# Kernel optimization log

Measured on AMD Instinct MI355X. Metric: run time of the kernel, lower is better.

The kernel has to match this reference:

```python
import jax, jax.numpy as jnp
import numpy as np

NSAMPLES = 30
TOPK = 32
EPS = 1e-8


def setup_inputs() -> dict:
    key = jax.random.key(0)
    k1, k2 = jax.random.split(key)
    B, N, C, S = 4, 4096, 256, 256
    x = jax.random.normal(k1, (B, N, C), dtype=jnp.float32)
    # affinity matrix (B, num_spixels, N); strictly positive weights for multinomial
    amatrix = jax.random.uniform(k2, (B, S, N), dtype=jnp.float32)
    return {"x": x, "amatrix": amatrix, "num_spixels": S}


def _exact_attn(x, sims, indices, labels):
    # x: (B,N,C); sims/indices: (B,S,K) topk affinities / pixel ids per superpixel
    # labels: (B,N) sampled superpixel id per pixel
    C = x.shape[-1]
    # per-pixel gather of its sampled superpixel's top-K member pixels
    idx = jnp.take_along_axis(indices, labels[:, :, None], axis=1)   # (B,N,K)
    w = jnp.take_along_axis(sims, labels[:, :, None], axis=1)        # (B,N,K)
    keys = jax.vmap(lambda xb, ib: xb[ib])(x, idx)                   # (B,N,K,C)
    scores = jnp.einsum('bnc,bnkc->bnk', x, keys) / jnp.sqrt(jnp.float32(C))
    attn = jax.nn.softmax(scores + jnp.log(w + EPS), axis=-1)        # (B,N,K)
    return jnp.einsum('bnk,bnkc->bnc', attn, keys)


def reference(x, amatrix, num_spixels):
    # topk over candidate-pixel axis, once (torch.topk(amatrix, topk, dim=-1))
    sims, indices = jax.lax.top_k(amatrix, TOPK)                     # (B,S,K)
    # multinomial(amatrix.T): sample a superpixel per pixel from its affinity column
    logits = jnp.log(amatrix + EPS).transpose(0, 2, 1)               # (B,N,S)
    sample_keys = jax.random.split(jax.random.key(1), NSAMPLES)

    def body(acc, k):
        labels = jax.random.categorical(k, logits, axis=-1)          # (B,N)
        acc = acc + _exact_attn(x, sims, indices, labels) / NSAMPLES
        return acc, None

    out, _ = jax.lax.scan(body, jnp.zeros_like(x), sample_keys)
    return out
```

## Files before the change

kernel.cpp:

```cpp
#include <hip/hip_runtime.h>
#include <hip/hip_bf16.h>


#define BB 4
#define NN 4096
#define CC 256
#define SS 256
#define KKK 32
#define NSAMP 30
#define NBIN (BB*SS)
#define TOTQ (NSAMP*BB*NN)

typedef _Float16 half8 __attribute__((ext_vector_type(8)));
typedef _Float16 half4v __attribute__((ext_vector_type(4)));
typedef float f32x4 __attribute__((ext_vector_type(4)));

struct Keys30 { unsigned k0[NSAMP]; unsigned k1[NSAMP]; };

__host__ __device__ __forceinline__ void threefry2x32(unsigned k0, unsigned k1,
    unsigned x0, unsigned x1, unsigned& o0, unsigned& o1) {
  unsigned ks2 = k0 ^ k1 ^ 0x1BD11BDAu;
#define TFROT(r) { x0 += x1; x1 = (x1 << (r)) | (x1 >> (32 - (r))); x1 ^= x0; }
  x0 += k0; x1 += k1;
  TFROT(13) TFROT(15) TFROT(26) TFROT(6)
  x0 += k1;  x1 += ks2 + 1u;
  TFROT(17) TFROT(29) TFROT(16) TFROT(24)
  x0 += ks2; x1 += k0 + 2u;
  TFROT(13) TFROT(15) TFROT(26) TFROT(6)
  x0 += k0;  x1 += k1 + 3u;
  TFROT(17) TFROT(29) TFROT(16) TFROT(24)
  x0 += k1;  x1 += ks2 + 4u;
  TFROT(13) TFROT(15) TFROT(26) TFROT(6)
  x0 += ks2; x1 += k0 + 5u;
#undef TFROT
  o0 = x0; o1 = x1;
}

__device__ __forceinline__ float gumbel_from_bits(unsigned bits) {
  float u = __uint_as_float((bits >> 9) | 0x3f800000u) - 1.0f;
  u = fmaxf(u, 1.17549435e-38f);
  return -logf(-logf(u));
}

__global__ __launch_bounds__(256) void logit_kernel(const float* __restrict__ am,
                                                    float* __restrict__ lg) {
  int i = (blockIdx.x * 256 + threadIdx.x) << 2;
  float4 v = *(const float4*)&am[i];
  float4 o;
  o.x = logf(v.x + 1e-8f); o.y = logf(v.y + 1e-8f);
  o.z = logf(v.z + 1e-8f); o.w = logf(v.w + 1e-8f);
  *(float4*)&lg[i] = o;
}

__global__ __launch_bounds__(256) void topk_kernel(const float* __restrict__ am,
                                                   int* __restrict__ indices,
                                                   float* __restrict__ logw) {
  __shared__ float vals[NN];
  __shared__ float wv[4];
  __shared__ int   wi[4];
  const int row = blockIdx.x;
  const int tid = threadIdx.x;
  const float* src = am + (size_t)row * NN;
  for (int i = tid; i < NN; i += 256) vals[i] = src[i];
  __syncthreads();
  for (int k = 0; k < KKK; ++k) {
    float bv = -INFINITY; int bi = -1;
    #pragma unroll
    for (int j = 0; j < NN / 256; ++j) {
      int idx = tid + j * 256;
      float v = vals[idx];
      if (v > bv) { bv = v; bi = idx; }
    }
    #pragma unroll
    for (int off = 32; off; off >>= 1) {
      float ov = __shfl_down(bv, off);
      int   oi = __shfl_down(bi, off);
      if (ov > bv || (ov == bv && oi < bi)) { bv = ov; bi = oi; }
    }
    if ((tid & 63) == 0) { wv[tid >> 6] = bv; wi[tid >> 6] = bi; }
    __syncthreads();
    if (tid == 0) {
      bv = wv[0]; bi = wi[0];
      for (int w = 1; w < 4; ++w)
        if (wv[w] > bv || (wv[w] == bv && wi[w] < bi)) { bv = wv[w]; bi = wi[w]; }
      indices[row * KKK + k] = bi;
      logw[row * KKK + k] = logf(bv + 1e-8f);
      vals[bi] = -INFINITY;
    }
    __syncthreads();
  }
}

__global__ __launch_bounds__(256) void sample_part_kernel(
    const float* __restrict__ lg, unsigned char* __restrict__ labels, Keys30 keys) {
  const int t = blockIdx.x * 256 + threadIdx.x;
  const int n = t & (NN - 1);
  const int b = (t >> 12) & 3;
  const int samp = t >> 14;
  const unsigned k0 = keys.k0[samp], k1 = keys.k1[samp];
  const unsigned jbase = ((unsigned)((b << 12) + n)) << 8;
  float best = -INFINITY; int bi = 0;
  for (int s = 0; s < SS; ++s) {
    float logit = lg[((b << 8) + s) * NN + n];
    unsigned o0, o1;
    threefry2x32(k0, k1, 0u, jbase + (unsigned)s, o0, o1);
    float tot = gumbel_from_bits(o0 ^ o1) + logit;
    if (tot > best) { best = tot; bi = s; }
  }
  labels[((samp << 2) + b) * NN + n] = (unsigned char)bi;
}

__global__ __launch_bounds__(256) void hist_kernel(const unsigned char* __restrict__ lbl,
                                                   int* __restrict__ hist) {
  __shared__ int h[NBIN];
  for (int i = threadIdx.x; i < NBIN; i += 256) h[i] = 0;
  __syncthreads();
  for (int e = blockIdx.x * 256 + threadIdx.x; e < TOTQ; e += gridDim.x * 256) {
    int bgrp = (e >> 12) & 3;
    atomicAdd(&h[(bgrp << 8) + lbl[e]], 1);
  }
  __syncthreads();
  for (int i = threadIdx.x; i < NBIN; i += 256) if (h[i]) atomicAdd(&hist[i], h[i]);
}

__global__ __launch_bounds__(1024) void scan_kernel(const int* __restrict__ hist,
                                                    int* __restrict__ binstart,
                                                    int* __restrict__ cursor) {
  __shared__ int a[NBIN];
  const int tid = threadIdx.x;
  const int h = hist[tid];
  a[tid] = h;
  __syncthreads();
  for (int off = 1; off < NBIN; off <<= 1) {
    int v = (tid >= off) ? a[tid - off] : 0;
    __syncthreads();
    a[tid] += v;
    __syncthreads();
  }
  int excl = a[tid] - h;
  binstart[tid] = excl;
  cursor[tid]   = excl;
}

__global__ __launch_bounds__(256) void scatter_kernel(const unsigned char* __restrict__ lbl,
                                                      int* __restrict__ cursor,
                                                      int* __restrict__ qlist) {
  for (int e = blockIdx.x * 256 + threadIdx.x; e < TOTQ; e += gridDim.x * 256) {
    int bgrp = (e >> 12) & 3;
    int bin = (bgrp << 8) + lbl[e];
    int slot = atomicAdd(&cursor[bin], 1);
    qlist[slot] = e & (NN - 1);
  }
}

__global__ __launch_bounds__(256, 2) void attn_mfma_kernel(
    const float* __restrict__ x, const int* __restrict__ indices,
    const float* __restrict__ logw, const int* __restrict__ qlist,
    const int* __restrict__ binstart, const int* __restrict__ hist,
    float* __restrict__ out) {
  __shared__ _Float16 Qlds[64 * 256];
  __shared__ _Float16 Klds[32 * 256];
  __shared__ _Float16 KT[256 * 40];
  __shared__ _Float16 Plds[4 * 16 * 32];
  __shared__ int   kidx_s[KKK];
  __shared__ float kbias_s[KKK];

  const int tid = threadIdx.x;
  const int b = blockIdx.x & 3;
  const int s = blockIdx.x >> 2;
  const int bin = (b << 8) + s;
  const int base = binstart[bin];
  const int cnt  = hist[bin];

  if (tid < KKK) {
    int r = bin * KKK + tid;
    kidx_s[tid]  = indices[r];
    kbias_s[tid] = logw[r];
  }
  __syncthreads();

  const int w = tid >> 6, lane = tid & 63;
  const int qr = lane & 15, kg = lane >> 4;

  {
    const int c4 = (lane) << 2;
    #pragma unroll
    for (int p = 0; p < 8; ++p) {
      int r = (p << 2) + w;
      const float4 v = *(const float4*)&x[((size_t)((b << 12) + kidx_s[r]) << 8) + c4];
      half4v h;
      h[0] = (_Float16)v.x; h[1] = (_Float16)v.y;
      h[2] = (_Float16)v.z; h[3] = (_Float16)v.w;
      *(half4v*)&Klds[(r << 8) + (c4 ^ ((r & 7) << 3))] = h;
      KT[(c4 + 0) * 40 + r] = h[0];
      KT[(c4 + 1) * 40 + r] = h[1];
      KT[(c4 + 2) * 40 + r] = h[2];
      KT[(c4 + 3) * 40 + r] = h[3];
    }
  }

  const int nchunk = (cnt + 63) >> 6;
  for (int chk = 0; chk < nchunk; ++chk) {
    const int rmax = min(64, cnt - (chk << 6));
    __syncthreads();
    {
      const int c4 = lane << 2;
      #pragma unroll
      for (int p = 0; p < 16; ++p) {
        int r = (p << 2) + w;
        int rr = min(r, rmax - 1);
        int n = qlist[base + (chk << 6) + rr];
        const float4 v = *(const float4*)&x[((size_t)((b << 12) + n) << 8) + c4];
        half4v h;
        h[0] = (_Float16)v.x; h[1] = (_Float16)v.y;
        h[2] = (_Float16)v.z; h[3] = (_Float16)v.w;
        *(half4v*)&Qlds[(r << 8) + (c4 ^ ((r & 7) << 3))] = h;
      }
    }
    __syncthreads();

    f32x4 acc0 = {0.f, 0.f, 0.f, 0.f}, acc1 = {0.f, 0.f, 0.f, 0.f};
    {
      const int arow = (w << 4) + qr;
      const _Float16* Arow = &Qlds[arow << 8];
      const int asz = (arow & 7) << 3;
      const _Float16* B0 = &Klds[qr << 8];
      const _Float16* B1 = &Klds[(16 + qr) << 8];
      const int bsz = (qr & 7) << 3;
      #pragma unroll
      for (int kk = 0; kk < 8; ++kk) {
        const int off = (kk << 5) + (kg << 3);
        half8 a  = *(const half8*)&Arow[off ^ asz];
        half8 b0 = *(const half8*)&B0[off ^ bsz];
        half8 b1 = *(const half8*)&B1[off ^ bsz];
        acc0 = __builtin_amdgcn_mfma_f32_16x16x32_f16(a, b0, acc0, 0, 0, 0);
        acc1 = __builtin_amdgcn_mfma_f32_16x16x32_f16(a, b1, acc1, 0, 0, 0);
      }
    }
    {
      const float b0v = kbias_s[qr], b1v = kbias_s[16 + qr];
      #pragma unroll
      for (int r = 0; r < 4; ++r) {
        float s0 = acc0[r] * 0.0625f + b0v;
        float s1 = acc1[r] * 0.0625f + b1v;
        float m = fmaxf(s0, s1);
        #pragma unroll
        for (int o = 1; o < 16; o <<= 1) m = fmaxf(m, __shfl_xor(m, o));
        float e0 = __expf(s0 - m), e1 = __expf(s1 - m);
        float sm = e0 + e1;
        #pragma unroll
        for (int o = 1; o < 16; o <<= 1) sm += __shfl_xor(sm, o);
        float inv = 1.0f / sm;
        int prow = (kg << 2) + r;
        _Float16* P = &Plds[(w << 9) + (prow << 5)];
        P[qr]      = (_Float16)(e0 * inv);
        P[16 + qr] = (_Float16)(e1 * inv);
      }
    }
    __builtin_amdgcn_wave_barrier();
    {
      half8 a2 = *(const half8*)&Plds[(w << 9) + (qr << 5) + (kg << 3)];
      int nr[4];
      #pragma unroll
      for (int r = 0; r < 4; ++r) {
        int grow = (w << 4) + (kg << 2) + r;
        nr[r] = (grow < rmax) ? qlist[base + (chk << 6) + grow] : -1;
      }
      #pragma unroll
      for (int t = 0; t < 16; ++t) {
        half8 bb = *(const half8*)&KT[((t << 4) + qr) * 40 + (kg << 3)];
        f32x4 zero = {0.f, 0.f, 0.f, 0.f};
        f32x4 o = __builtin_amdgcn_mfma_f32_16x16x32_f16(a2, bb, zero, 0, 0, 0);
        #pragma unroll
        for (int r = 0; r < 4; ++r) {
          if (nr[r] >= 0)
            atomicAdd(&out[((size_t)((b << 12) + nr[r]) << 8) + (t << 4) + qr],
                      o[r] * (1.0f / 30.0f));
        }
      }
    }
  }
}

#define OFF_IDX   0
#define OFF_LOGW  131072
#define OFF_LBL   262144
#define OFF_LOGIT 786432
#define OFF_HIST  17563648
#define OFF_BST   17567744
#define OFF_CUR   17571840
#define OFF_QL    17575936

extern "C" void kernel_launch(void* const* d_in, const int* in_sizes, int n_in,
                              void* d_out, int out_size, void* d_ws, size_t ws_size,
                              hipStream_t stream) {
  const float* x  = (const float*)d_in[0];
  const float* am = (const float*)d_in[1];
  float* out = (float*)d_out;

  char* ws = (char*)d_ws;
  int*   indices = (int*)(ws + OFF_IDX);
  float* logw    = (float*)(ws + OFF_LOGW);
  unsigned char* labels = (unsigned char*)(ws + OFF_LBL);
  float* logits  = (float*)(ws + OFF_LOGIT);
  int*   hist    = (int*)(ws + OFF_HIST);
  int*   binstart= (int*)(ws + OFF_BST);
  int*   cursor  = (int*)(ws + OFF_CUR);
  int*   qlist   = (int*)(ws + OFF_QL);

  Keys30 keys;
  for (int s = 0; s < NSAMP; ++s) {
    unsigned o0, o1;
    threefry2x32(0u, 1u, 0u, (unsigned)s, o0, o1);
    keys.k0[s] = o0; keys.k1[s] = o1;
  }

  hipMemsetAsync(d_out, 0, (size_t)out_size * 4, stream);
  hipMemsetAsync(hist, 0, NBIN * 4, stream);

  logit_kernel<<<(BB * SS * NN) / (256 * 4), 256, 0, stream>>>(am, logits);
  topk_kernel<<<BB * SS, 256, 0, stream>>>(am, indices, logw);
  sample_part_kernel<<<TOTQ / 256, 256, 0, stream>>>(logits, labels, keys);
  hist_kernel<<<240, 256, 0, stream>>>(labels, hist);
  scan_kernel<<<1, 1024, 0, stream>>>(hist, binstart, cursor);
  scatter_kernel<<<240, 256, 0, stream>>>(labels, cursor, qlist);
  attn_mfma_kernel<<<NBIN, 256, 0, stream>>>(x, indices, logw, qlist, binstart,
                                             hist, out);
}
```

Baseline: 998.0 us.

## Screen Gumbel-max candidates with fast logs, recompute exact only near-best

The sampling kernel now scores each candidate superpixel with fast __logf Gumbel noise and keeps a running threshold. It marks only candidates within a small margin of the running best, or with extreme noise, and re-evaluates just those with exact logf to choose the argmax. This targets the cost of two precise logs per candidate across all 256 superpixels. In exchange it adds a second threefry evaluation per surviving candidate plus divergent per-wave loops, and it relies on the margin to preserve exact label selection. The rotate is also expressed as a builtin.

```diff
diff --git a/kernel.cpp b/kernel.cpp
--- a/kernel.cpp
+++ b/kernel.cpp
@@ -20,7 +20,7 @@
 __host__ __device__ __forceinline__ void threefry2x32(unsigned k0, unsigned k1,
     unsigned x0, unsigned x1, unsigned& o0, unsigned& o1) {
   unsigned ks2 = k0 ^ k1 ^ 0x1BD11BDAu;
-#define TFROT(r) { x0 += x1; x1 = (x1 << (r)) | (x1 >> (32 - (r))); x1 ^= x0; }
+#define TFROT(r) { x0 += x1; x1 = __builtin_rotateleft32(x1, (r)); x1 ^= x0; }
   x0 += k0; x1 += k1;
   TFROT(13) TFROT(15) TFROT(26) TFROT(6)
   x0 += k1;  x1 += ks2 + 1u;
@@ -36,9 +36,13 @@
   o0 = x0; o1 = x1;
 }
 
-__device__ __forceinline__ float gumbel_from_bits(unsigned bits) {
+__device__ __forceinline__ float uniform_from_bits(unsigned bits) {
   float u = __uint_as_float((bits >> 9) | 0x3f800000u) - 1.0f;
-  u = fmaxf(u, 1.17549435e-38f);
+  return fmaxf(u, 1.17549435e-38f);
+}
+
+__device__ __forceinline__ float gumbel_exact(unsigned bits) {
+  float u = uniform_from_bits(bits);
   return -logf(-logf(u));
 }
 
@@ -91,7 +95,7 @@
   }
 }
 
-__global__ __launch_bounds__(256) void sample_part_kernel(
+__global__ __launch_bounds__(256) void sample_screen_kernel(
     const float* __restrict__ lg, unsigned char* __restrict__ labels, Keys30 keys) {
   const int t = blockIdx.x * 256 + threadIdx.x;
   const int n = t & (NN - 1);
@@ -99,13 +103,40 @@
   const int samp = t >> 14;
   const unsigned k0 = keys.k0[samp], k1 = keys.k1[samp];
   const unsigned jbase = ((unsigned)((b << 12) + n)) << 8;
-  float best = -INFINITY; int bi = 0;
-  for (int s = 0; s < SS; ++s) {
-    float logit = lg[((b << 8) + s) * NN + n];
-    unsigned o0, o1;
-    threefry2x32(k0, k1, 0u, jbase + (unsigned)s, o0, o1);
-    float tot = gumbel_from_bits(o0 ^ o1) + logit;
-    if (tot > best) { best = tot; bi = s; }
+  const float* lcol = lg + ((size_t)(b << 8)) * NN + n;
+
+  const float MARGIN2 = 0.01f;
+  float thr  = -INFINITY;
+  float best = -INFINITY;
+  int   bi   = 0;
+
+  for (int grp = 0; grp < 8; ++grp) {
+    const int sbase = grp << 5;
+    unsigned m = 0;
+    #pragma unroll 4
+    for (int i = 0; i < 32; ++i) {
+      const int s = sbase + i;
+      float logit = lcol[(size_t)s * NN];
+      unsigned o0, o1;
+      threefry2x32(k0, k1, 0u, jbase + (unsigned)s, o0, o1);
+      float u  = uniform_from_bits(o0 ^ o1);
+      float gt = -__logf(-__logf(u));
+      float at = gt + logit;
+      bool force = (gt > 16.0f) || !(gt == gt);
+      if (force || at >= thr - MARGIN2) m |= (1u << i);
+      if (!force) thr = fmaxf(thr, at);
+    }
+    while (__ballot(m != 0)) {
+      if (m) {
+        int i = __builtin_ctz(m);
+        m &= m - 1;
+        int s = sbase + i;
+        unsigned o0, o1;
+        threefry2x32(k0, k1, 0u, jbase + (unsigned)s, o0, o1);
+        float tot = gumbel_exact(o0 ^ o1) + lcol[(size_t)s * NN];
+        if (tot > best) { best = tot; bi = s; }
+      }
+    }
   }
   labels[((samp << 2) + b) * NN + n] = (unsigned char)bi;
 }
@@ -320,7 +351,7 @@
 
   logit_kernel<<<(BB * SS * NN) / (256 * 4), 256, 0, stream>>>(am, logits);
   topk_kernel<<<BB * SS, 256, 0, stream>>>(am, indices, logw);
-  sample_part_kernel<<<TOTQ / 256, 256, 0, stream>>>(logits, labels, keys);
+  sample_screen_kernel<<<TOTQ / 256, 256, 0, stream>>>(logits, labels, keys);
   hist_kernel<<<240, 256, 0, stream>>>(labels, hist);
   scan_kernel<<<1, 1024, 0, stream>>>(hist, binstart, cursor);
   scatter_kernel<<<240, 256, 0, stream>>>(labels, cursor, qlist);
```

New measurement: 1.042 ms. 4.4% more time.

## Replace Gumbel double-log sampling with exponential-race using one fast log

Applied to the files above, without the earlier changes.

Sampling now uses the identity argmax(g+log w) = argmin(-log u / w), so each candidate costs one hardware log and a multiply by a precomputed -1/w, instead of two accurate logs plus a logit add. The kernel tracks the best and second-best ratio and, when the two are within a small relative margin, redoes the exact Gumbel computation so the chosen labels match the reference. The rotate macro now uses a rotate builtin. The risk is the fallback path causing wavefront divergence, and the approximate log possibly picking a different winner at ties outside the guard margin.

```diff
diff --git a/kernel.cpp b/kernel.cpp
--- a/kernel.cpp
+++ b/kernel.cpp
@@ -20,7 +20,7 @@
 __host__ __device__ __forceinline__ void threefry2x32(unsigned k0, unsigned k1,
     unsigned x0, unsigned x1, unsigned& o0, unsigned& o1) {
   unsigned ks2 = k0 ^ k1 ^ 0x1BD11BDAu;
-#define TFROT(r) { x0 += x1; x1 = (x1 << (r)) | (x1 >> (32 - (r))); x1 ^= x0; }
+#define TFROT(r) { x0 += x1; x1 = __builtin_rotateleft32(x1, (r)); x1 ^= x0; }
   x0 += k0; x1 += k1;
   TFROT(13) TFROT(15) TFROT(26) TFROT(6)
   x0 += k1;  x1 += ks2 + 1u;
@@ -36,20 +36,24 @@
   o0 = x0; o1 = x1;
 }
 
-__device__ __forceinline__ float gumbel_from_bits(unsigned bits) {
+__device__ __forceinline__ float uniform_from_bits(unsigned bits) {
   float u = __uint_as_float((bits >> 9) | 0x3f800000u) - 1.0f;
-  u = fmaxf(u, 1.17549435e-38f);
+  return fmaxf(u, 1.17549435e-38f);
+}
+
+__device__ __forceinline__ float gumbel_exact(unsigned bits) {
+  float u = uniform_from_bits(bits);
   return -logf(-logf(u));
 }
 
-__global__ __launch_bounds__(256) void logit_kernel(const float* __restrict__ am,
-                                                    float* __restrict__ lg) {
+__global__ __launch_bounds__(256) void invw_kernel(const float* __restrict__ am,
+                                                   float* __restrict__ nw) {
   int i = (blockIdx.x * 256 + threadIdx.x) << 2;
   float4 v = *(const float4*)&am[i];
   float4 o;
-  o.x = logf(v.x + 1e-8f); o.y = logf(v.y + 1e-8f);
-  o.z = logf(v.z + 1e-8f); o.w = logf(v.w + 1e-8f);
-  *(float4*)&lg[i] = o;
+  o.x = -1.0f / (v.x + 1e-8f); o.y = -1.0f / (v.y + 1e-8f);
+  o.z = -1.0f / (v.z + 1e-8f); o.w = -1.0f / (v.w + 1e-8f);
+  *(float4*)&nw[i] = o;
 }
 
 __global__ __launch_bounds__(256) void topk_kernel(const float* __restrict__ am,
@@ -91,23 +95,45 @@
   }
 }
 
-__global__ __launch_bounds__(256) void sample_part_kernel(
-    const float* __restrict__ lg, unsigned char* __restrict__ labels, Keys30 keys) {
-  const int t = blockIdx.x * 256 + threadIdx.x;
-  const int n = t & (NN - 1);
-  const int b = (t >> 12) & 3;
-  const int samp = t >> 14;
+__global__ __launch_bounds__(256) void sample_top2_kernel(
+    const float* __restrict__ ninvw, const float* __restrict__ am,
+    unsigned char* __restrict__ labels, Keys30 keys) {
+  const int t0 = blockIdx.x * 256 + threadIdx.x;
+  const int n = t0 & (NN - 1);
+  const int b = (t0 >> 12) & 3;
+  const int samp = t0 >> 14;
   const unsigned k0 = keys.k0[samp], k1 = keys.k1[samp];
   const unsigned jbase = ((unsigned)((b << 12) + n)) << 8;
-  float best = -INFINITY; int bi = 0;
+  const float* wcol = ninvw + ((size_t)(b << 8)) * NN + n;
+
+  float r1 = INFINITY, r2 = INFINITY;
+  int   i1 = 0;
+  #pragma unroll 8
   for (int s = 0; s < SS; ++s) {
-    float logit = lg[((b << 8) + s) * NN + n];
     unsigned o0, o1;
     threefry2x32(k0, k1, 0u, jbase + (unsigned)s, o0, o1);
-    float tot = gumbel_from_bits(o0 ^ o1) + logit;
-    if (tot > best) { best = tot; bi = s; }
-  }
-  labels[((samp << 2) + b) * NN + n] = (unsigned char)bi;
+    float u = uniform_from_bits(o0 ^ o1);
+    float r = __builtin_amdgcn_logf(u) * wcol[(size_t)s * NN];
+    bool better = r < r1;
+    r2 = better ? r1 : fminf(r2, r);
+    r1 = better ? r  : r1;
+    i1 = better ? s  : i1;
+  }
+  bool uncert = !(r2 > r1 * 1.0001f);
+  if (__ballot(uncert)) {
+    if (uncert) {
+      const float* acol = am + ((size_t)(b << 8)) * NN + n;
+      float best = -INFINITY; int bi = 0;
+      for (int s = 0; s < SS; ++s) {
+        unsigned o0, o1;
+        threefry2x32(k0, k1, 0u, jbase + (unsigned)s, o0, o1);
+        float tot = gumbel_exact(o0 ^ o1) + logf(acol[(size_t)s * NN] + 1e-8f);
+        if (tot > best) { best = tot; bi = s; }
+      }
+      i1 = bi;
+    }
+  }
+  labels[((samp << 2) + b) * NN + n] = (unsigned char)i1;
 }
 
 __global__ __launch_bounds__(256) void hist_kernel(const unsigned char* __restrict__ lbl,
@@ -285,7 +311,7 @@
 #define OFF_IDX   0
 #define OFF_LOGW  131072
 #define OFF_LBL   262144
-#define OFF_LOGIT 786432
+#define OFF_NW    786432
 #define OFF_HIST  17563648
 #define OFF_BST   17567744
 #define OFF_CUR   17571840
@@ -302,7 +328,7 @@
   int*   indices = (int*)(ws + OFF_IDX);
   float* logw    = (float*)(ws + OFF_LOGW);
   unsigned char* labels = (unsigned char*)(ws + OFF_LBL);
-  float* logits  = (float*)(ws + OFF_LOGIT);
+  float* ninvw   = (float*)(ws + OFF_NW);
   int*   hist    = (int*)(ws + OFF_HIST);
   int*   binstart= (int*)(ws + OFF_BST);
   int*   cursor  = (int*)(ws + OFF_CUR);
@@ -318,9 +344,9 @@
   hipMemsetAsync(d_out, 0, (size_t)out_size * 4, stream);
   hipMemsetAsync(hist, 0, NBIN * 4, stream);
 
-  logit_kernel<<<(BB * SS * NN) / (256 * 4), 256, 0, stream>>>(am, logits);
+  invw_kernel<<<(BB * SS * NN) / (256 * 4), 256, 0, stream>>>(am, ninvw);
   topk_kernel<<<BB * SS, 256, 0, stream>>>(am, indices, logw);
-  sample_part_kernel<<<TOTQ / 256, 256, 0, stream>>>(logits, labels, keys);
+  sample_top2_kernel<<<TOTQ / 256, 256, 0, stream>>>(ninvw, am, labels, keys);
   hist_kernel<<<240, 256, 0, stream>>>(labels, hist);
   scan_kernel<<<1, 1024, 0, stream>>>(hist, binstart, cursor);
   scatter_kernel<<<240, 256, 0, stream>>>(labels, cursor, qlist);
```

New measurement: 1.047 ms. 4.9% more time.
